# Performance work log

Hardware: AMD Instinct MI355X
Metric: run time of the kernel (lower is better)

The kernel has to match this reference:

```python
import jax, jax.numpy as jnp
import numpy as np

B, N, D = 2, 2048, 1024
H = 16
HD = D // H  # 64
N_CTX = 256


def setup_inputs() -> dict:
    key = jax.random.key(0)
    ks = jax.random.split(key, 10)
    x = jax.random.normal(ks[0], (B, N, D), dtype=jnp.float32)
    ctx_ppr = jax.random.uniform(ks[1], (N_CTX,), dtype=jnp.float32, minval=1e-4, maxval=1.0)
    ctx_trust = jax.random.uniform(ks[2], (N_CTX,), dtype=jnp.float32)
    attn_mask = jax.random.randint(ks[3], (N, N), 0, 2).astype(jnp.bool_)
    # parameters (nn.Linear convention: y = x @ W.T + b)
    s_in = 1.0 / np.sqrt(D)
    W_in = jax.random.uniform(ks[4], (3 * D, D), dtype=jnp.float32, minval=-s_in, maxval=s_in)
    b_in = jax.random.uniform(ks[5], (3 * D,), dtype=jnp.float32, minval=-s_in, maxval=s_in)
    W_out = jax.random.uniform(ks[6], (D, D), dtype=jnp.float32, minval=-s_in, maxval=s_in)
    b_out = jax.random.uniform(ks[7], (D,), dtype=jnp.float32, minval=-s_in, maxval=s_in)
    log_ppr_alpha = jnp.ones((1,), jnp.float32) * 0.1
    trust_scale = jnp.ones((1,), jnp.float32) * 0.1
    return {"x": x, "ctx_ppr": ctx_ppr, "ctx_trust": ctx_trust, "n_ctx": N_CTX,
            "attn_mask": attn_mask, "W_in": W_in, "b_in": b_in,
            "W_out": W_out, "b_out": b_out,
            "log_ppr_alpha": log_ppr_alpha, "trust_scale": trust_scale}


def reference(x, ctx_ppr, ctx_trust, n_ctx, attn_mask, W_in, b_in, W_out, b_out,
              log_ppr_alpha, trust_scale):
    Bx, Nx, Dx = x.shape
    scale = HD ** -0.5
    qkv = x @ W_in.T + b_in  # [B,N,3D]
    q, k, v = jnp.split(qkv, 3, axis=-1)
    q = q.reshape(Bx, Nx, H, HD).transpose(0, 2, 1, 3)  # [B,H,N,d]
    k = k.reshape(Bx, Nx, H, HD).transpose(0, 2, 1, 3)
    v = v.reshape(Bx, Nx, H, HD).transpose(0, 2, 1, 3)
    if n_ctx > 0:
        gate = jax.nn.sigmoid(trust_scale[0] * ctx_trust)  # [n_ctx]
        gate_full = jnp.concatenate([gate, jnp.ones(Nx - n_ctx, x.dtype)])
        v = v * gate_full[None, None, :, None]
    logits = jnp.einsum('bhqd,bhkd->bhqk', q, k) * scale
    if n_ctx > 0:
        bias = log_ppr_alpha[0] * jnp.log(jnp.clip(ctx_ppr, 1e-8, None))
        col_bias = jnp.concatenate([bias, jnp.zeros(Nx - n_ctx, x.dtype)])
        logits = logits + col_bias[None, None, None, :]
    logits = jnp.where(attn_mask[None, None, :, :], -jnp.inf, logits)
    weights = jax.nn.softmax(logits, axis=-1)
    out = jnp.einsum('bhqk,bhkd->bhqd', weights, v)
    out = out.transpose(0, 2, 1, 3).reshape(Bx, Nx, Dx)
    return out @ W_out.T + b_out
```

## Files before the change

### kernel.cpp

```cpp
#include <hip/hip_runtime.h>
#include <hip/hip_bf16.h>
#include <hip/hip_fp16.h>
#include <math.h>

#define B_   2
#define N_   2048
#define D_   1024
#define H_   16
#define TD_  3072
#define LOG2E 1.44269504088896340736f
#define SCALE_Q (0.125f * LOG2E)

typedef short  bf16x8 __attribute__((ext_vector_type(8)));
typedef _Float16 f16x8 __attribute__((ext_vector_type(8)));
typedef float  f32x4  __attribute__((ext_vector_type(4)));
typedef float  f32x16 __attribute__((ext_vector_type(16)));

#define MFMA16(a, b, c)   __builtin_amdgcn_mfma_f32_16x16x32_bf16(a, b, c, 0, 0, 0)
#define MFMA32B(a, b, c)  __builtin_amdgcn_mfma_f32_32x32x16_bf16(a, b, c, 0, 0, 0)
#define MFMA32H(a, b, c)  __builtin_amdgcn_mfma_f32_32x32x16_f16(a, b, c, 0, 0, 0)

__device__ __forceinline__ ushort f2bf(float f) {
    union { float f; unsigned u; } v; v.f = f;
    unsigned r = (v.u + 0x7fffu + ((v.u >> 16) & 1u)) >> 16;
    return (ushort)r;
}
__device__ __forceinline__ unsigned pkrtz(float a, float b) {
    typedef __fp16 h2 __attribute__((ext_vector_type(2)));
    union { h2 h; unsigned u; } c;
    c.h = __builtin_amdgcn_cvt_pkrtz(a, b);
    return c.u;
}
__device__ __forceinline__ void async16(const void* g, void* l) {
    __builtin_amdgcn_global_load_lds(
        (const __attribute__((address_space(1))) unsigned*)g,
        (__attribute__((address_space(3))) unsigned*)l, 16, 0, 0);
}

__global__ __launch_bounds__(256) void preprocess(
    const float* __restrict__ x, const float* __restrict__ W_in,
    const float* __restrict__ W_out, const float* __restrict__ ctx_ppr,
    const float* __restrict__ log_alpha, const int* __restrict__ n_ctx_p,
    const int* __restrict__ mask,
    ushort* __restrict__ xb, ushort* __restrict__ wib, ushort* __restrict__ wob,
    float* __restrict__ term)
{
    const int J0 = 1048576, J1 = 786432, J2 = 262144, JT = 1048576;
    int t = blockIdx.x * 256 + threadIdx.x;
    if (t < J0 + J1 + J2) {
        const float* src; ushort* dst; int i = t;
        if (i < J0)           { src = x;      dst = xb;  }
        else if (i < J0 + J1) { i -= J0;      src = W_in;  dst = wib; }
        else                  { i -= J0 + J1; src = W_out; dst = wob; }
        float4 v = ((const float4*)src)[i];
        ushort4 o;
        o.x = f2bf(v.x); o.y = f2bf(v.y); o.z = f2bf(v.z); o.w = f2bf(v.w);
        ((ushort4*)dst)[i] = o;
    } else if (t < J0 + J1 + J2 + JT) {
        int i = t - (J0 + J1 + J2);
        int k4 = (i & 511) * 4;
        int4 m = ((const int4*)mask)[i];
        int nc = n_ctx_p[0];
        float al = log_alpha[0];
        float4 o;
        float bv[4];
        #pragma unroll
        for (int j = 0; j < 4; ++j) {
            int k = k4 + j;
            bv[j] = (k < nc) ? (al * __log2f(fmaxf(ctx_ppr[k], 1e-8f)) - 4.f) : -4.f;
        }
        o.x = m.x ? -1e30f : bv[0];
        o.y = m.y ? -1e30f : bv[1];
        o.z = m.z ? -1e30f : bv[2];
        o.w = m.w ? -1e30f : bv[3];
        ((float4*)term)[i] = o;
    }
}

template<int BCOL, int MODE>
__global__ __launch_bounds__(256) void gemm_bt(
    const ushort* __restrict__ A, const ushort* __restrict__ Bw,
    const float* __restrict__ bias, float* __restrict__ Cf,
    ushort* __restrict__ Ch, int Ncol, int K,
    const float* __restrict__ ctx_trust, const float* __restrict__ trust_scale,
    const int* __restrict__ n_ctx_p)
{
    constexpr int NT = BCOL / 32;
    __shared__ ushort tA[128 * 32];
    __shared__ ushort tB[BCOL * 32];
    const int tid = threadIdx.x;
    const int lane = tid & 63, wv = tid >> 6;
    const int ln = lane & 15, kg = lane >> 4;
    const int rh = wv >> 1, ch = wv & 1;
    const int row0 = blockIdx.y * 128, col0 = blockIdx.x * BCOL;

    int offA[4], offB[NT];
    #pragma unroll
    for (int i = 0; i < 4; ++i) {
        int ra = rh * 64 + i * 16 + ln;
        offA[i] = ra * 32 + ((kg ^ ((ra >> 1) & 3)) << 3);
    }
    #pragma unroll
    for (int i = 0; i < NT; ++i) {
        int rb = ch * (BCOL / 2) + i * 16 + ln;
        offB[i] = rb * 32 + ((kg ^ ((rb >> 1) & 3)) << 3);
    }
    f32x4 acc[4][NT];
    #pragma unroll
    for (int i = 0; i < 4; ++i)
        #pragma unroll
        for (int j = 0; j < NT; ++j) acc[i][j] = (f32x4){0.f, 0.f, 0.f, 0.f};

    for (int kt = 0; kt < K; kt += 32) {
        __syncthreads();
        #pragma unroll
        for (int r2 = 0; r2 < 2; ++r2) {
            int g = r2 * 256 + tid;
            int row = g >> 2;
            int srck = ((g & 3) ^ ((row >> 1) & 3)) << 3;
            async16(A + (size_t)(row0 + row) * K + kt + srck, &tA[g * 8]);
        }
        #pragma unroll
        for (int r2 = 0; r2 < BCOL / 64; ++r2) {
            int g = r2 * 256 + tid;
            int row = g >> 2;
            int srck = ((g & 3) ^ ((row >> 1) & 3)) << 3;
            async16(Bw + (size_t)(col0 + row) * K + kt + srck, &tB[g * 8]);
        }
        __syncthreads();
        bf16x8 af[4], bfr[NT];
        #pragma unroll
        for (int i = 0; i < 4; ++i)  af[i]  = *(const bf16x8*)&tA[offA[i]];
        #pragma unroll
        for (int i = 0; i < NT; ++i) bfr[i] = *(const bf16x8*)&tB[offB[i]];
        #pragma unroll
        for (int mt = 0; mt < 4; ++mt)
            #pragma unroll
            for (int nt = 0; nt < NT; ++nt)
                acc[mt][nt] = MFMA16(af[mt], bfr[nt], acc[mt][nt]);
    }

    const int nctx = n_ctx_p ? n_ctx_p[0] : 0;
    const float ts = trust_scale ? trust_scale[0] : 0.f;
    #pragma unroll
    for (int nt = 0; nt < NT; ++nt) {
        int col = col0 + ch * (BCOL / 2) + nt * 16 + ln;
        float cbv = (MODE != 2) ? bias[col] : 0.f;
        float gmul = 1.f;
        if (MODE == 2) {
            int tok = col & (N_ - 1);
            if (tok < nctx)
                gmul = 1.f / (1.f + __expf(-ts * ctx_trust[tok]));
        }
        #pragma unroll
        for (int mt = 0; mt < 4; ++mt) {
            int rbase = row0 + rh * 64 + mt * 16 + kg * 4;
            f32x4 a = acc[mt][nt];
            if (MODE == 0) {
                #pragma unroll
                for (int reg = 0; reg < 4; ++reg)
                    Cf[(size_t)(rbase + reg) * Ncol + col] = a[reg] + cbv;
            } else if (MODE == 1) {
                const float qs = (col < D_) ? SCALE_Q : 1.f;
                #pragma unroll
                for (int reg = 0; reg < 4; ++reg)
                    Ch[(size_t)(rbase + reg) * Ncol + col] = f2bf((a[reg] + cbv) * qs);
            } else {
                f32x4 bv4 = *(const f32x4*)&bias[rbase];
                #pragma unroll
                for (int reg = 0; reg < 4; ++reg) {
                    float v = (a[reg] + bv4[reg]) * gmul;
                    _Float16 hv = (_Float16)v;
                    union { _Float16 h; ushort u; } cv; cv.h = hv;
                    Ch[((size_t)((col >> 11) * 1024 + rbase + reg)) * 2048 + (col & (N_ - 1))] = cv.u;
                }
            }
        }
    }
}

__global__ __launch_bounds__(512, 4) void attn(
    const ushort* __restrict__ qkb,
    const _Float16* __restrict__ vT,
    const float* __restrict__ term,
    float* __restrict__ pO,
    float* __restrict__ pl)
{
    __shared__ ushort   Kt[2][64 * 64];
    __shared__ _Float16 Vt[2][64 * 64];
    const int tid = threadIdx.x;
    const int lane = tid & 63, wv = tid >> 6;
    const int q31 = lane & 31, hi = lane >> 5;
    const int bh = blockIdx.x;
    const int b = bh >> 4, h = bh & 15;
    const int z = blockIdx.z;
    const int k0z = z * 1024;
    const int q = blockIdx.y * 256 + wv * 32 + q31;

    bf16x8 qf[4];
    {
        const ushort* qrow = qkb + (size_t)(b * N_ + q) * 2048 + h * 64;
        #pragma unroll
        for (int ks = 0; ks < 4; ++ks)
            qf[ks] = *(const bf16x8*)(qrow + ks * 16 + hi * 8);
    }
    const size_t kgbase = (size_t)(b * N_) * 2048 + 1024 + h * 64;
    const _Float16* vbase = vT + (size_t)(b * 1024 + h * 64) * 2048;
    const float* trow = term + (size_t)q * 2048 + k0z;

    f32x16 O[2];
    O[0] = (f32x16)(0.f); O[1] = (f32x16)(0.f);
    float lrun = 0.f;

    {
        int g = tid; int row = g >> 3;
        int sg = (g & 7) ^ ((row ^ (row >> 3)) & 7);
        async16(qkb + kgbase + (size_t)(k0z + row) * 2048 + sg * 8, &Kt[0][g * 8]);
        async16(vbase + (size_t)row * 2048 + k0z + sg * 8, &Vt[0][g * 8]);
    }

    int fsw[2];
    #pragma unroll
    for (int t = 0; t < 2; ++t) {
        int row = t * 32 + q31;
        fsw[t] = (row ^ (row >> 3)) & 7;
    }

    for (int ci = 0; ci < 16; ++ci) {
        const int c0 = ci * 64;
        __syncthreads();
        if (ci < 15) {
            const int c1 = c0 + 64, nb = (ci + 1) & 1;
            int g = tid; int row = g >> 3;
            int sg = (g & 7) ^ ((row ^ (row >> 3)) & 7);
            async16(qkb + kgbase + (size_t)(k0z + c1 + row) * 2048 + sg * 8, &Kt[nb][g * 8]);
            async16(vbase + (size_t)row * 2048 + k0z + c1 + sg * 8, &Vt[nb][g * 8]);
        }
        const ushort*   KT = Kt[ci & 1];
        const _Float16* VT = Vt[ci & 1];

        f32x4 tm[2][4];
        #pragma unroll
        for (int t = 0; t < 2; ++t)
            #pragma unroll
            for (int g = 0; g < 4; ++g)
                tm[t][g] = *(const f32x4*)(trow + c0 + t * 32 + g * 8 + hi * 4);

        f32x16 S[2];
        S[0] = (f32x16)(0.f); S[1] = (f32x16)(0.f);
        #pragma unroll
        for (int t = 0; t < 2; ++t) {
            const int rbase = (t * 32 + q31) * 64;
            #pragma unroll
            for (int ks = 0; ks < 4; ++ks) {
                bf16x8 kf = *(const bf16x8*)&KT[rbase + (((ks * 2 + hi) ^ fsw[t]) << 3)];
                S[t] = MFMA32B(kf, qf[ks], S[t]);
            }
        }

        unsigned pk[2][8];
        __half2 hs0 = __float2half2_rn(0.f), hs1 = __float2half2_rn(0.f);
        #pragma unroll
        for (int t = 0; t < 2; ++t) {
            float p[16];
            #pragma unroll
            for (int g = 0; g < 4; ++g)
                #pragma unroll
                for (int r = 0; r < 4; ++r) {
                    const int reg = g * 4 + r;
                    p[reg] = __builtin_exp2f(S[t][reg] + tm[t][g][r]);
                }
            #pragma unroll
            for (int i = 0; i < 8; ++i) {
                pk[t][i] = pkrtz(p[2 * i], p[2 * i + 1]);
                union { unsigned u; __half2 h; } c; c.u = pk[t][i];
                if (i & 1) hs1 = __hadd2(hs1, c.h); else hs0 = __hadd2(hs0, c.h);
            }
        }
        {
            __half2 hs = __hadd2(hs0, hs1);
            lrun += __low2float(hs) + __high2float(hs);
        }

        #pragma unroll
        for (int ks = 0; ks < 4; ++ks) {
            const int t = ks >> 1, lo4 = (ks & 1) * 4;
            unsigned u0 = pk[t][lo4 + 0], u1 = pk[t][lo4 + 1];
            unsigned u2 = pk[t][lo4 + 2], u3 = pk[t][lo4 + 3];
            unsigned own0 = hi ? u2 : u0, own1 = hi ? u3 : u1;
            unsigned snd0 = hi ? u0 : u2, snd1 = hi ? u1 : u3;
            unsigned rv0 = (unsigned)__shfl_xor((int)snd0, 32);
            unsigned rv1 = (unsigned)__shfl_xor((int)snd1, 32);
            union { f16x8 v; unsigned u[4]; } frag;
            frag.u[0] = hi ? rv0 : own0;
            frag.u[1] = hi ? rv1 : own1;
            frag.u[2] = hi ? own0 : rv0;
            frag.u[3] = hi ? own1 : rv1;
            #pragma unroll
            for (int t2 = 0; t2 < 2; ++t2) {
                const int vb = (t2 * 32 + q31) * 64;
                union { f16x8 v; int4 i; } vf;
                vf.i = *(const int4*)&VT[vb + (((ks * 2 + hi) ^ fsw[t2]) << 3)];
                O[t2] = MFMA32H(vf.v, frag.v, O[t2]);
            }
        }
    }

    float* obase = pO + (((size_t)(z * 32 + bh) * 2048) + q) * 64;
    #pragma unroll
    for (int t = 0; t < 2; ++t)
        #pragma unroll
        for (int g = 0; g < 4; ++g) {
            f32x4 o4 = { O[t][g * 4 + 0], O[t][g * 4 + 1], O[t][g * 4 + 2], O[t][g * 4 + 3] };
            *(f32x4*)(obase + t * 32 + g * 8 + hi * 4) = o4;
        }
    float l = lrun + __shfl_xor(lrun, 32);
    if (hi == 0)
        pl[(size_t)(z * 32 + bh) * 2048 + q] = l;
}

__global__ __launch_bounds__(256) void combine(
    const float* __restrict__ pO, const float* __restrict__ pl,
    ushort* __restrict__ attb)
{
    int i = blockIdx.x * 256 + threadIdx.x;
    int bhq = i >> 4, d4 = (i & 15) << 2;
    const float* o0 = pO + (size_t)bhq * 64 + d4;
    const float* o1 = o0 + (size_t)32 * 2048 * 64;
    float l = pl[bhq] + pl[bhq + 32 * 2048];
    float inv = 1.f / l;
    f32x4 a = *(const f32x4*)o0;
    f32x4 b = *(const f32x4*)o1;
    ushort4 o;
    #pragma unroll
    for (int r = 0; r < 4; ++r)
        ((ushort*)&o)[r] = f2bf((a[r] + b[r]) * inv);
    int bh = bhq >> 11, q = bhq & 2047;
    *(ushort4*)&attb[((size_t)((bh >> 4) * 2048 + q)) * 1024 + (bh & 15) * 64 + d4] = o;
}

extern "C" void kernel_launch(void* const* d_in, const int* in_sizes, int n_in,
                              void* d_out, int out_size, void* d_ws, size_t ws_size,
                              hipStream_t stream)
{
    const float* x         = (const float*)d_in[0];
    const float* ctx_ppr   = (const float*)d_in[1];
    const float* ctx_trust = (const float*)d_in[2];
    const int*   n_ctx_p   = (const int*)d_in[3];
    const int*   attn_mask = (const int*)d_in[4];
    const float* W_in      = (const float*)d_in[5];
    const float* b_in      = (const float*)d_in[6];
    const float* W_out     = (const float*)d_in[7];
    const float* b_out     = (const float*)d_in[8];
    const float* log_alpha = (const float*)d_in[9];
    const float* trust_sc  = (const float*)d_in[10];
    float* out = (float*)d_out;

    char* ws = (char*)d_ws;
    ushort*    xb     = (ushort*)ws;    ws += (size_t)4096 * 1024 * 2;
    ushort*    wib    = (ushort*)ws;    ws += (size_t)3072 * 1024 * 2;
    ushort*    wob    = (ushort*)ws;    ws += (size_t)1024 * 1024 * 2;
    ushort*    qkb    = (ushort*)ws;    ws += (size_t)4096 * 2048 * 2;
    _Float16*  vT     = (_Float16*)ws;  ws += (size_t)2048 * 2048 * 2;
    ushort*    attbuf = (ushort*)ws;    ws += (size_t)4096 * 1024 * 2;
    float*     term   = (float*)ws;     ws += (size_t)2048 * 2048 * 4;
    float*     pO     = (float*)ws;     ws += (size_t)2 * 32 * 2048 * 64 * 4;
    float*     pl     = (float*)ws;     ws += (size_t)2 * 32 * 2048 * 4;

    hipLaunchKernelGGL(preprocess, dim3(12288), dim3(256), 0, stream,
                       x, W_in, W_out, ctx_ppr, log_alpha, n_ctx_p, attn_mask,
                       xb, wib, wob, term);

    hipLaunchKernelGGL((gemm_bt<128, 1>), dim3(16, 32), dim3(256), 0, stream,
                       xb, wib, b_in, (float*)nullptr, qkb, 2048, 1024,
                       (const float*)nullptr, (const float*)nullptr, (const int*)nullptr);

    hipLaunchKernelGGL((gemm_bt<64, 2>), dim3(64, 8), dim3(256), 0, stream,
                       wib + (size_t)2048 * 1024, xb, b_in + 2 * D_, (float*)nullptr,
                       (ushort*)vT, 4096, 1024, ctx_trust, trust_sc, n_ctx_p);

    hipLaunchKernelGGL(attn, dim3(32, 8, 2), dim3(512), 0, stream,
                       qkb, vT, term, pO, pl);

    hipLaunchKernelGGL(combine, dim3(4096), dim3(256), 0, stream,
                       pO, pl, attbuf);

    hipLaunchKernelGGL((gemm_bt<64, 0>), dim3(16, 32), dim3(256), 0, stream,
                       attbuf, wob, b_out, out, (ushort*)nullptr, 1024, 1024,
                       (const float*)nullptr, (const float*)nullptr, (const int*)nullptr);
}
```

Baseline: 269.1 us.

## Pack attention mask into bits and split keys four ways

Replaces the precomputed float bias+mask matrix (16MB read by every head) with a bitpacked mask plus a per-column bias row, which sharply cuts memory traffic in the attention kernel. The key-split factor goes from 2 to 4, doubling the attention grid for better CU occupancy, and combine now reduces four partials. Workspace is re-laid so pO aliases the bf16 input buffers to fit the larger partial arrays. The cost is extra partial-output traffic and per-element bit tests in the softmax loop.

```diff
diff --git a/kernel.cpp b/kernel.cpp
--- a/kernel.cpp
+++ b/kernel.cpp
@@ -43,9 +43,9 @@
     const float* __restrict__ log_alpha, const int* __restrict__ n_ctx_p,
     const int* __restrict__ mask,
     ushort* __restrict__ xb, ushort* __restrict__ wib, ushort* __restrict__ wob,
-    float* __restrict__ term)
+    float* __restrict__ biasrow, unsigned* __restrict__ maskbits)
 {
-    const int J0 = 1048576, J1 = 786432, J2 = 262144, JT = 1048576;
+    const int J0 = 1048576, J1 = 786432, J2 = 262144, JM = 131072, JB = 2048;
     int t = blockIdx.x * 256 + threadIdx.x;
     if (t < J0 + J1 + J2) {
         const float* src; ushort* dst; int i = t;
@@ -56,24 +56,25 @@
         ushort4 o;
         o.x = f2bf(v.x); o.y = f2bf(v.y); o.z = f2bf(v.z); o.w = f2bf(v.w);
         ((ushort4*)dst)[i] = o;
-    } else if (t < J0 + J1 + J2 + JT) {
+    } else if (t < J0 + J1 + J2 + JM) {
         int i = t - (J0 + J1 + J2);
-        int k4 = (i & 511) * 4;
-        int4 m = ((const int4*)mask)[i];
+        const int4* m = (const int4*)(mask + (size_t)i * 32);
+        unsigned bits = 0u;
+        #pragma unroll
+        for (int j = 0; j < 8; ++j) {
+            int4 w = m[j];
+            bits |= (w.x != 0 ? 1u : 0u) << (j * 4 + 0);
+            bits |= (w.y != 0 ? 1u : 0u) << (j * 4 + 1);
+            bits |= (w.z != 0 ? 1u : 0u) << (j * 4 + 2);
+            bits |= (w.w != 0 ? 1u : 0u) << (j * 4 + 3);
+        }
+        maskbits[i] = bits;
+    } else if (t < J0 + J1 + J2 + JM + JB) {
+        int k = t - (J0 + J1 + J2 + JM);
         int nc = n_ctx_p[0];
-        float al = log_alpha[0];
-        float4 o;
-        float bv[4];
-        #pragma unroll
-        for (int j = 0; j < 4; ++j) {
-            int k = k4 + j;
-            bv[j] = (k < nc) ? (al * __log2f(fmaxf(ctx_ppr[k], 1e-8f)) - 4.f) : -4.f;
-        }
-        o.x = m.x ? -1e30f : bv[0];
-        o.y = m.y ? -1e30f : bv[1];
-        o.z = m.z ? -1e30f : bv[2];
-        o.w = m.w ? -1e30f : bv[3];
-        ((float4*)term)[i] = o;
+        float bv = -4.f;
+        if (k < nc) bv = log_alpha[0] * __log2f(fmaxf(ctx_ppr[k], 1e-8f)) - 4.f;
+        biasrow[k] = bv;
     }
 }
 
@@ -182,7 +183,8 @@
 __global__ __launch_bounds__(512, 4) void attn(
     const ushort* __restrict__ qkb,
     const _Float16* __restrict__ vT,
-    const float* __restrict__ term,
+    const unsigned* __restrict__ maskbits,
+    const float* __restrict__ biasrow,
     float* __restrict__ pO,
     float* __restrict__ pl)
 {
@@ -194,7 +196,7 @@
     const int bh = blockIdx.x;
     const int b = bh >> 4, h = bh & 15;
     const int z = blockIdx.z;
-    const int k0z = z * 1024;
+    const int k0z = z * 512;
     const int q = blockIdx.y * 256 + wv * 32 + q31;
 
     bf16x8 qf[4];
@@ -206,7 +208,6 @@
     }
     const size_t kgbase = (size_t)(b * N_) * 2048 + 1024 + h * 64;
     const _Float16* vbase = vT + (size_t)(b * 1024 + h * 64) * 2048;
-    const float* trow = term + (size_t)q * 2048 + k0z;
 
     f32x16 O[2];
     O[0] = (f32x16)(0.f); O[1] = (f32x16)(0.f);
@@ -226,10 +227,10 @@
         fsw[t] = (row ^ (row >> 3)) & 7;
     }
 
-    for (int ci = 0; ci < 16; ++ci) {
+    for (int ci = 0; ci < 8; ++ci) {
         const int c0 = ci * 64;
         __syncthreads();
-        if (ci < 15) {
+        if (ci < 7) {
             const int c1 = c0 + 64, nb = (ci + 1) & 1;
             int g = tid; int row = g >> 3;
             int sg = (g & 7) ^ ((row ^ (row >> 3)) & 7);
@@ -239,12 +240,14 @@
         const ushort*   KT = Kt[ci & 1];
         const _Float16* VT = Vt[ci & 1];
 
-        f32x4 tm[2][4];
+        uint2 mw = *(const uint2*)&maskbits[(size_t)q * 64 + z * 16 + ci * 2];
+        unsigned msh[2] = { mw.x >> (hi * 4), mw.y >> (hi * 4) };
+        f32x4 bb[2][4];
         #pragma unroll
         for (int t = 0; t < 2; ++t)
             #pragma unroll
             for (int g = 0; g < 4; ++g)
-                tm[t][g] = *(const f32x4*)(trow + c0 + t * 32 + g * 8 + hi * 4);
+                bb[t][g] = *(const f32x4*)&biasrow[k0z + c0 + t * 32 + g * 8 + hi * 4];
 
         f32x16 S[2];
         S[0] = (f32x16)(0.f); S[1] = (f32x16)(0.f);
@@ -268,7 +271,10 @@
                 #pragma unroll
                 for (int r = 0; r < 4; ++r) {
                     const int reg = g * 4 + r;
-                    p[reg] = __builtin_exp2f(S[t][reg] + tm[t][g][r]);
+                    const int br = r + 8 * g;
+                    float s = S[t][reg] + bb[t][g][r];
+                    s = ((msh[t] >> br) & 1u) ? -1e30f : s;
+                    p[reg] = __builtin_exp2f(s);
                 }
             #pragma unroll
             for (int i = 0; i < 8; ++i) {
@@ -323,18 +329,20 @@
     const float* __restrict__ pO, const float* __restrict__ pl,
     ushort* __restrict__ attb)
 {
+    const size_t ZSTR = (size_t)32 * 2048 * 64;
     int i = blockIdx.x * 256 + threadIdx.x;
     int bhq = i >> 4, d4 = (i & 15) << 2;
     const float* o0 = pO + (size_t)bhq * 64 + d4;
-    const float* o1 = o0 + (size_t)32 * 2048 * 64;
-    float l = pl[bhq] + pl[bhq + 32 * 2048];
+    float l = pl[bhq] + pl[bhq + 65536] + pl[bhq + 131072] + pl[bhq + 196608];
     float inv = 1.f / l;
-    f32x4 a = *(const f32x4*)o0;
-    f32x4 b = *(const f32x4*)o1;
+    f32x4 a0 = *(const f32x4*)o0;
+    f32x4 a1 = *(const f32x4*)(o0 + ZSTR);
+    f32x4 a2 = *(const f32x4*)(o0 + 2 * ZSTR);
+    f32x4 a3 = *(const f32x4*)(o0 + 3 * ZSTR);
     ushort4 o;
     #pragma unroll
     for (int r = 0; r < 4; ++r)
-        ((ushort*)&o)[r] = f2bf((a[r] + b[r]) * inv);
+        ((ushort*)&o)[r] = f2bf(((a0[r] + a1[r]) + (a2[r] + a3[r])) * inv);
     int bh = bhq >> 11, q = bhq & 2047;
     *(ushort4*)&attb[((size_t)((bh >> 4) * 2048 + q)) * 1024 + (bh & 15) * 64 + d4] = o;
 }
@@ -357,19 +365,21 @@
     float* out = (float*)d_out;
 
     char* ws = (char*)d_ws;
-    ushort*    xb     = (ushort*)ws;    ws += (size_t)4096 * 1024 * 2;
-    ushort*    wib    = (ushort*)ws;    ws += (size_t)3072 * 1024 * 2;
-    ushort*    wob    = (ushort*)ws;    ws += (size_t)1024 * 1024 * 2;
+    float*     pO     = (float*)ws;
+    ushort*    xb     = (ushort*)ws;
+    ushort*    wib    = (ushort*)(ws + (size_t)4096 * 1024 * 2);
+    ws += (size_t)4 * 32 * 2048 * 64 * 4;
+    float*     pl     = (float*)ws;     ws += (size_t)4 * 32 * 2048 * 4;
     ushort*    qkb    = (ushort*)ws;    ws += (size_t)4096 * 2048 * 2;
     _Float16*  vT     = (_Float16*)ws;  ws += (size_t)2048 * 2048 * 2;
     ushort*    attbuf = (ushort*)ws;    ws += (size_t)4096 * 1024 * 2;
-    float*     term   = (float*)ws;     ws += (size_t)2048 * 2048 * 4;
-    float*     pO     = (float*)ws;     ws += (size_t)2 * 32 * 2048 * 64 * 4;
-    float*     pl     = (float*)ws;     ws += (size_t)2 * 32 * 2048 * 4;
-
-    hipLaunchKernelGGL(preprocess, dim3(12288), dim3(256), 0, stream,
+    ushort*    wob    = (ushort*)ws;    ws += (size_t)1024 * 1024 * 2;
+    unsigned*  maskbits = (unsigned*)ws; ws += (size_t)2048 * 64 * 4;
+    float*     biasrow  = (float*)ws;    ws += 2048 * 4;
+
+    hipLaunchKernelGGL(preprocess, dim3(8712), dim3(256), 0, stream,
                        x, W_in, W_out, ctx_ppr, log_alpha, n_ctx_p, attn_mask,
-                       xb, wib, wob, term);
+                       xb, wib, wob, biasrow, maskbits);
 
     hipLaunchKernelGGL((gemm_bt<128, 1>), dim3(16, 32), dim3(256), 0, stream,
                        xb, wib, b_in, (float*)nullptr, qkb, 2048, 1024,
@@ -379,8 +389,8 @@
                        wib + (size_t)2048 * 1024, xb, b_in + 2 * D_, (float*)nullptr,
                        (ushort*)vT, 4096, 1024, ctx_trust, trust_sc, n_ctx_p);
 
-    hipLaunchKernelGGL(attn, dim3(32, 8, 2), dim3(512), 0, stream,
-                       qkb, vT, term, pO, pl);
+    hipLaunchKernelGGL(attn, dim3(32, 8, 4), dim3(512), 0, stream,
+                       qkb, vT, maskbits, biasrow, pO, pl);
 
     hipLaunchKernelGGL(combine, dim3(4096), dim3(256), 0, stream,
                        pO, pl, attbuf);
```

New measurement: 277.8 us. 1.03x slower.
